# Kernel tuning notes

Hardware: AMD Instinct MI355X
Metric: run time of the kernel (lower is better)

Reference implementation:

```python
import jax, jax.numpy as jnp
import numpy as np

B, S, HID = 1, 2048, 4096
NH, KVH, D = 32, 8, 128
MAXP = 2048
EPS = 1e-6


def _rope_tables(max_pos, dim, base=10000.0):
    inv_freq = 1.0 / (base ** (np.arange(0, dim, 2, dtype=np.float32) / dim))
    t = np.arange(max_pos, dtype=np.float32)
    freqs = np.outer(t, inv_freq)                      # [max_pos, dim/2]
    emb = np.concatenate([freqs, freqs], axis=-1)      # [max_pos, dim]
    return jnp.asarray(np.cos(emb)), jnp.asarray(np.sin(emb))


def setup_inputs() -> dict:
    key = jax.random.key(0)
    ks = jax.random.split(key, 6)
    x = jax.random.normal(ks[0], (B, S, HID), jnp.float32)
    scale = 0.02
    wq = jax.random.normal(ks[1], (NH * D, HID), jnp.float32) * scale
    wk = jax.random.normal(ks[2], (KVH * D, HID), jnp.float32) * scale
    wv = jax.random.normal(ks[3], (KVH * D, HID), jnp.float32) * scale
    wo = jax.random.normal(ks[4], (NH * D, HID), jnp.float32).T * scale  # stored as [HID, NH*D] -> transpose back
    wo = jnp.asarray(jax.random.normal(ks[4], (HID, NH * D), jnp.float32) * scale)
    cos_table, sin_table = _rope_tables(MAXP, D)
    return {
        "x": x, "wq": wq, "wk": wk, "wv": wv, "wo": wo,
        "q_norm_w": jnp.ones((D,), jnp.float32),
        "k_norm_w": jnp.ones((D,), jnp.float32),
        "cos_table": cos_table, "sin_table": sin_table,
        "k_cache": jnp.zeros((1, B, MAXP, KVH, D), jnp.float32),
        "v_cache": jnp.zeros((1, B, MAXP, KVH, D), jnp.float32),
        "positions": jnp.arange(S, dtype=jnp.int32),
        "layer_idx": 0,
    }


def _rmsnorm(x, w):
    return w * (x * jax.lax.rsqrt(jnp.mean(x * x, axis=-1, keepdims=True) + EPS))


def _rope(x, cos, sin):
    # x: [B, H, S, D]; cos/sin: [1, 1, S, D]
    half = x.shape[-1] // 2
    x1, x2 = x[..., :half], x[..., half:]
    rotated = jnp.concatenate([-x2, x1], axis=-1)
    return x * cos + rotated * sin


def reference(x, wq, wk, wv, wo, q_norm_w, k_norm_w, cos_table, sin_table,
              k_cache, v_cache, positions, layer_idx):
    bsz, seq_len, _ = x.shape
    d = q_norm_w.shape[0]
    nh = wq.shape[0] // d
    kvh = wk.shape[0] // d
    g = nh // kvh

    q = (x @ wq.T).reshape(bsz, seq_len, nh, d).transpose(0, 2, 1, 3)    # [B,NH,S,D]
    k = (x @ wk.T).reshape(bsz, seq_len, kvh, d).transpose(0, 2, 1, 3)   # [B,KVH,S,D]
    v = (x @ wv.T).reshape(bsz, seq_len, kvh, d).transpose(0, 2, 1, 3)

    q = _rmsnorm(q, q_norm_w)
    k = _rmsnorm(k, k_norm_w)

    cos = cos_table[positions][None, None]  # [1,1,S,D]
    sin = sin_table[positions][None, None]
    q = _rope(q, cos, sin)
    k = _rope(k, cos, sin)

    # KV-cache scatter at dynamic positions (prefill: positions = arange(S))
    kc = k_cache[layer_idx].at[:, positions].set(k.transpose(0, 2, 1, 3))
    vc = v_cache[layer_idx].at[:, positions].set(v.transpose(0, 2, 1, 3))
    # K = max(positions)+1 == seq_len in this (prefill) setup; static for jit
    K = seq_len
    k_all = kc[:, :K].transpose(0, 2, 1, 3)   # [B,KVH,K,D]
    v_all = vc[:, :K].transpose(0, 2, 1, 3)

    # GQA: group query heads instead of repeat_interleave on K/V (same math)
    qg = q.reshape(bsz, kvh, g, seq_len, d)
    scale = 1.0 / jnp.sqrt(jnp.asarray(d, q.dtype))
    scores = jnp.einsum('bkgqd,bkld->bkgql', qg, k_all) * scale
    causal = jnp.tril(jnp.ones((seq_len, K), dtype=bool))
    scores = jnp.where(causal, scores, jnp.finfo(scores.dtype).min)
    attn = jax.nn.softmax(scores, axis=-1)
    out = jnp.einsum('bkgql,bkld->bkgqd', attn, v_all)
    out = out.reshape(bsz, nh, seq_len, d).transpose(0, 2, 1, 3).reshape(bsz, seq_len, nh * d)
    return out @ wo.T
```

## Files before the change

### kernel.cpp

```cpp
#include <hip/hip_runtime.h>

typedef unsigned short u16;
typedef unsigned int u32;
typedef __attribute__((ext_vector_type(8))) short bf16x8;
typedef __attribute__((ext_vector_type(4))) float f32x4;
struct __align__(8) us4 { u16 x, y, z, w; };

#define S_LEN 2048
#define HID   4096
#define NH    32
#define KVH   8
#define HD    128
#define MFMA16 __builtin_amdgcn_mfma_f32_16x16x32_bf16

__device__ inline u16 f2bf(float f) {
  u32 u = __float_as_uint(f);
  u32 r = (u + 0x7fffu + ((u >> 16) & 1u)) >> 16;
  return (u16)r;
}
__device__ inline float bf2f(u16 h) { return __uint_as_float(((u32)h) << 16); }

__device__ inline void gld_lds16(const void* g, void* l) {
  __builtin_amdgcn_global_load_lds(
      (const __attribute__((address_space(1))) u32*)g,
      (__attribute__((address_space(3))) u32*)l, 16, 0, 0);
}

__global__ __launch_bounds__(256)
void cvt_all(const float* __restrict__ x, const float* __restrict__ wq,
             const float* __restrict__ wk, const float* __restrict__ wv,
             u16* __restrict__ xb, u16* __restrict__ wqkvb) {
  int b = blockIdx.x;
  const float* in; u16* out; int base;
  if (b < 8192)       { in = x;  out = xb;                    base = b; }
  else if (b < 24576) { in = wq; out = wqkvb;                 base = b - 8192; }
  else if (b < 28672) { in = wk; out = wqkvb + 16777216;      base = b - 24576; }
  else                { in = wv; out = wqkvb + 20971520;      base = b - 28672; }
  size_t i = ((size_t)base * 256 + threadIdx.x) * 4;
  f32x4 v = *(const f32x4*)(in + i);
  us4 o;
  o.x = f2bf(v[0]); o.y = f2bf(v[1]); o.z = f2bf(v[2]); o.w = f2bf(v[3]);
  *(us4*)(out + i) = o;
}

__device__ __forceinline__ void stage_slab(const u16* __restrict__ src, int ldk,
                                           int rowBase, int k0, char* lslot,
                                           int t) {
  int rl = t >> 3;
  int c8 = ((t & 7) ^ (rl & 7)) * 8;
  gld_lds16(src + (size_t)(rowBase + rl) * ldk + k0 + c8, lslot + t * 16);
}

__device__ __forceinline__ void stage_half(const u16* __restrict__ src, int ldk,
                                           int rowBase, int k0, char* lslot,
                                           int t) {
  int rl = t >> 3;
  int c8 = ((t & 7) ^ (rl & 7)) * 8;
  gld_lds16(src + (size_t)(rowBase + rl) * ldk + k0 + c8, lslot + t * 16);
  gld_lds16(src + (size_t)(rowBase + 64 + rl) * ldk + k0 + c8,
            lslot + 8192 + t * 16);
}

__global__ __launch_bounds__(512, 2)
void gemm_qkv8(const u16* __restrict__ xb, const u16* __restrict__ wqkvb,
               u16* __restrict__ Qp, u16* __restrict__ Kp, u16* __restrict__ vt) {
  extern __shared__ char lds[];
  const int id = blockIdx.x;
  const int sw = (id & 7) * 32 + (id >> 3);
  const int by = sw >> 5, bx = sw & 31;
  const int m0 = by * 256, n0 = bx * 192;
  const int t = threadIdx.x;
  const int l = t & 63, w = t >> 6;
  const int l15 = l & 15, quad = l >> 4;
  const int wr = w >> 1, wcn = w & 1;
  char* ldsA = lds;
  char* ldsB = lds + 65536;
  const int swz0 = ((0 + quad) ^ (l15 & 7)) * 16;
  const int swz1 = ((4 + quad) ^ (l15 & 7)) * 16;
  const int aB0 = wr * 8192 + l15 * 128;
  const int bB0 = wcn * 12288 + l15 * 128;
  const int nt = HID / 64;

  f32x4 acc[4][6];
#pragma unroll
  for (int m = 0; m < 4; m++)
#pragma unroll
    for (int n = 0; n < 6; n++) acc[m][n] = (f32x4){0.f, 0.f, 0.f, 0.f};

#pragma unroll
  for (int s = 0; s < 3; s++) stage_slab(wqkvb, HID, n0 + s * 64, 0, ldsB + s * 8192, t);
#pragma unroll
  for (int s = 0; s < 4; s++) stage_slab(xb, HID, m0 + s * 64, 0, ldsA + s * 8192, t);
#pragma unroll
  for (int s = 0; s < 3; s++) stage_slab(wqkvb, HID, n0 + s * 64, 64, ldsB + 24576 + s * 8192, t);
  asm volatile("s_waitcnt vmcnt(3)" ::: "memory");
  __builtin_amdgcn_s_barrier();

  bf16x8 a[2][2], a2[2][2], b[3][2], b2[3][2];
#pragma unroll 1
  for (int tt = 0; tt < nt; ++tt) {
    const int d = tt & 1, dn = d ^ 1;
    const int aO = d * 32768 + aB0;
    const int bO = d * 24576 + bB0;
    const int k1 = (tt + 1) * 64, k2 = (tt + 2) * 64;
    const bool pf1 = (tt + 1 < nt), pf2 = (tt + 2 < nt);

#pragma unroll
    for (int m = 0; m < 2; m++) {
      a[m][0] = *(const bf16x8*)(ldsA + aO + m * 2048 + swz0);
      a[m][1] = *(const bf16x8*)(ldsA + aO + m * 2048 + swz1);
    }
#pragma unroll
    for (int n = 0; n < 3; n++) {
      b[n][0] = *(const bf16x8*)(ldsB + bO + n * 2048 + swz0);
      b[n][1] = *(const bf16x8*)(ldsB + bO + n * 2048 + swz1);
    }
    if (pf1) {
      stage_slab(xb, HID, m0,      k1, ldsA + dn * 32768,        t);
      stage_slab(xb, HID, m0 + 64, k1, ldsA + dn * 32768 + 8192, t);
    }
    __builtin_amdgcn_s_barrier();
    __builtin_amdgcn_s_setprio(1);
#pragma unroll
    for (int m = 0; m < 2; m++)
#pragma unroll
      for (int n = 0; n < 3; n++) {
        acc[m][n] = MFMA16(a[m][0], b[n][0], acc[m][n], 0, 0, 0);
        acc[m][n] = MFMA16(a[m][1], b[n][1], acc[m][n], 0, 0, 0);
      }
    __builtin_amdgcn_s_setprio(0);
    __builtin_amdgcn_s_barrier();

#pragma unroll
    for (int n = 0; n < 3; n++) {
      b2[n][0] = *(const bf16x8*)(ldsB + bO + (3 + n) * 2048 + swz0);
      b2[n][1] = *(const bf16x8*)(ldsB + bO + (3 + n) * 2048 + swz1);
    }
    if (pf1) {
      stage_slab(xb, HID, m0 + 128, k1, ldsA + dn * 32768 + 16384, t);
      stage_slab(xb, HID, m0 + 192, k1, ldsA + dn * 32768 + 24576, t);
    }
    __builtin_amdgcn_s_barrier();
    __builtin_amdgcn_s_setprio(1);
#pragma unroll
    for (int m = 0; m < 2; m++)
#pragma unroll
      for (int n = 0; n < 3; n++) {
        acc[m][3 + n] = MFMA16(a[m][0], b2[n][0], acc[m][3 + n], 0, 0, 0);
        acc[m][3 + n] = MFMA16(a[m][1], b2[n][1], acc[m][3 + n], 0, 0, 0);
      }
    __builtin_amdgcn_s_setprio(0);
    __builtin_amdgcn_s_barrier();

#pragma unroll
    for (int m = 0; m < 2; m++) {
      a2[m][0] = *(const bf16x8*)(ldsA + aO + (2 + m) * 2048 + swz0);
      a2[m][1] = *(const bf16x8*)(ldsA + aO + (2 + m) * 2048 + swz1);
    }
    if (pf2) {
#pragma unroll
      for (int s = 0; s < 3; s++)
        stage_slab(wqkvb, HID, n0 + s * 64, k2, ldsB + d * 24576 + s * 8192, t);
    }
    __builtin_amdgcn_s_barrier();
    __builtin_amdgcn_s_setprio(1);
#pragma unroll
    for (int m = 0; m < 2; m++)
#pragma unroll
      for (int n = 0; n < 3; n++) {
        acc[2 + m][n] = MFMA16(a2[m][0], b[n][0], acc[2 + m][n], 0, 0, 0);
        acc[2 + m][n] = MFMA16(a2[m][1], b[n][1], acc[2 + m][n], 0, 0, 0);
      }
#pragma unroll
    for (int m = 0; m < 2; m++)
#pragma unroll
      for (int n = 0; n < 3; n++) {
        acc[2 + m][3 + n] = MFMA16(a2[m][0], b2[n][0], acc[2 + m][3 + n], 0, 0, 0);
        acc[2 + m][3 + n] = MFMA16(a2[m][1], b2[n][1], acc[2 + m][3 + n], 0, 0, 0);
      }
    __builtin_amdgcn_s_setprio(0);
    if (pf1) {
      if (pf2) asm volatile("s_waitcnt vmcnt(3)" ::: "memory");
      else     asm volatile("s_waitcnt vmcnt(0)" ::: "memory");
      __builtin_amdgcn_s_barrier();
    }
  }

#pragma unroll
  for (int m = 0; m < 4; m++) {
    int row0 = m0 + wr * 64 + m * 16 + quad * 4;
#pragma unroll
    for (int n = 0; n < 6; n++) {
      int col = n0 + wcn * 96 + n * 16 + l15;
      if (col < 4096) {
#pragma unroll
        for (int r = 0; r < 4; r++)
          Qp[(size_t)(row0 + r) * HID + col] = f2bf(acc[m][n][r]);
      } else if (col < 5120) {
#pragma unroll
        for (int r = 0; r < 4; r++)
          Kp[(size_t)(row0 + r) * 1024 + (col - 4096)] = f2bf(acc[m][n][r]);
      } else {
        us4 v;
        v.x = f2bf(acc[m][n][0]); v.y = f2bf(acc[m][n][1]);
        v.z = f2bf(acc[m][n][2]); v.w = f2bf(acc[m][n][3]);
        *(us4*)(vt + (size_t)(col - 5120) * S_LEN + row0) = v;
      }
    }
  }
}

__device__ __forceinline__ void gemm256_core(
    const u16* __restrict__ A, const u16* __restrict__ W, int m0, int n0,
    int ldk, int kBeg, int kEnd, char* lds, f32x4 (&acc)[8][4]) {
  const int t = threadIdx.x;
  const int l = t & 63, w = t >> 6;
  const int l15 = l & 15, quad = l >> 4;
  const int wr = w >> 2, wcn = w & 3;
  const int nt = (kEnd - kBeg) >> 6;
  char* ldsA = lds;
  char* ldsB = lds + 65536;
  const int swz0 = ((0 + quad) ^ (l15 & 7)) * 16;
  const int swz1 = ((4 + quad) ^ (l15 & 7)) * 16;
  const int aB0 = wr * 16384 + l15 * 128;
  const int bB0 = wcn * 8192 + l15 * 128;

#pragma unroll
  for (int m = 0; m < 8; m++)
#pragma unroll
    for (int n = 0; n < 4; n++) acc[m][n] = (f32x4){0.f, 0.f, 0.f, 0.f};

  stage_half(W, ldk, n0,       kBeg, ldsB,         t);
  stage_half(W, ldk, n0 + 128, kBeg, ldsB + 16384, t);
  stage_half(A, ldk, m0,       kBeg, ldsA,         t);
  stage_half(A, ldk, m0 + 128, kBeg, ldsA + 16384, t);
  if (nt > 1) {
    stage_half(W, ldk, n0,       kBeg + 64, ldsB + 32768,         t);
    stage_half(W, ldk, n0 + 128, kBeg + 64, ldsB + 32768 + 16384, t);
    stage_half(A, ldk, m0,       kBeg + 64, ldsA + 32768,         t);
    stage_half(A, ldk, m0 + 128, kBeg + 64, ldsA + 32768 + 16384, t);
    asm volatile("s_waitcnt vmcnt(8)" ::: "memory");
  } else {
    asm volatile("s_waitcnt vmcnt(0)" ::: "memory");
  }
  __builtin_amdgcn_s_barrier();

  bf16x8 a[4][2], b[2][2], b2[2][2];
#pragma unroll 1
  for (int tt = 0; tt < nt; ++tt) {
    const int d = tt & 1;
    const int aO = d * 32768 + aB0;
    const int bO = d * 32768 + bB0;
    const int k2 = kBeg + (tt + 2) * 64;
    const bool pf = (tt + 2 < nt);

#pragma unroll
    for (int m = 0; m < 4; m++) {
      a[m][0] = *(const bf16x8*)(ldsA + aO + m * 2048 + swz0);
      a[m][1] = *(const bf16x8*)(ldsA + aO + m * 2048 + swz1);
    }
#pragma unroll
    for (int n = 0; n < 2; n++) {
      b[n][0] = *(const bf16x8*)(ldsB + bO + n * 2048 + swz0);
      b[n][1] = *(const bf16x8*)(ldsB + bO + n * 2048 + swz1);
    }
    __builtin_amdgcn_s_barrier();
    __builtin_amdgcn_s_setprio(1);
#pragma unroll
    for (int m = 0; m < 4; m++)
#pragma unroll
      for (int n = 0; n < 2; n++) {
        acc[m][n] = MFMA16(a[m][0], b[n][0], acc[m][n], 0, 0, 0);
        acc[m][n] = MFMA16(a[m][1], b[n][1], acc[m][n], 0, 0, 0);
      }
    __builtin_amdgcn_s_setprio(0);
    __builtin_amdgcn_s_barrier();

#pragma unroll
    for (int n = 0; n < 2; n++) {
      b2[n][0] = *(const bf16x8*)(ldsB + bO + (2 + n) * 2048 + swz0);
      b2[n][1] = *(const bf16x8*)(ldsB + bO + (2 + n) * 2048 + swz1);
    }
    __builtin_amdgcn_s_barrier();
    __builtin_amdgcn_s_setprio(1);
#pragma unroll
    for (int m = 0; m < 4; m++)
#pragma unroll
      for (int n = 0; n < 2; n++) {
        acc[m][2 + n] = MFMA16(a[m][0], b2[n][0], acc[m][2 + n], 0, 0, 0);
        acc[m][2 + n] = MFMA16(a[m][1], b2[n][1], acc[m][2 + n], 0, 0, 0);
      }
    __builtin_amdgcn_s_setprio(0);
    __builtin_amdgcn_s_barrier();

    if (pf) {
      stage_half(W, ldk, n0,       k2, ldsB + d * 32768,         t);
      stage_half(W, ldk, n0 + 128, k2, ldsB + d * 32768 + 16384, t);
    }
#pragma unroll
    for (int m = 0; m < 4; m++) {
      a[m][0] = *(const bf16x8*)(ldsA + aO + (4 + m) * 2048 + swz0);
      a[m][1] = *(const bf16x8*)(ldsA + aO + (4 + m) * 2048 + swz1);
    }
    __builtin_amdgcn_s_barrier();
    __builtin_amdgcn_s_setprio(1);
#pragma unroll
    for (int m = 0; m < 4; m++)
#pragma unroll
      for (int n = 0; n < 2; n++) {
        acc[4 + m][n] = MFMA16(a[m][0], b[n][0], acc[4 + m][n], 0, 0, 0);
        acc[4 + m][n] = MFMA16(a[m][1], b[n][1], acc[4 + m][n], 0, 0, 0);
      }
    __builtin_amdgcn_s_setprio(0);
    __builtin_amdgcn_s_barrier();

    if (pf) {
      stage_half(A, ldk, m0,       k2, ldsA + d * 32768,         t);
      stage_half(A, ldk, m0 + 128, k2, ldsA + d * 32768 + 16384, t);
    }
    __builtin_amdgcn_s_barrier();
    __builtin_amdgcn_s_setprio(1);
#pragma unroll
    for (int m = 0; m < 4; m++)
#pragma unroll
      for (int n = 0; n < 2; n++) {
        acc[4 + m][2 + n] = MFMA16(a[m][0], b2[n][0], acc[4 + m][2 + n], 0, 0, 0);
        acc[4 + m][2 + n] = MFMA16(a[m][1], b2[n][1], acc[4 + m][2 + n], 0, 0, 0);
      }
    __builtin_amdgcn_s_setprio(0);
    if (pf) asm volatile("s_waitcnt vmcnt(8)" ::: "memory");
    else    asm volatile("s_waitcnt vmcnt(0)" ::: "memory");
    __builtin_amdgcn_s_barrier();
  }
}

__global__ __launch_bounds__(512, 2)
void gemm_out8(const u16* __restrict__ ab, const u16* __restrict__ wob,
               float* __restrict__ O0, float* __restrict__ O1) {
  extern __shared__ char lds[];
  const int id = blockIdx.x;
  const int sw = (id & 7) * 32 + (id >> 3);
  const int z = sw >> 7, rem = sw & 127;
  const int by = rem >> 4, bx = rem & 15;
  float* Op = z ? O1 : O0;

  f32x4 acc[8][4];
  gemm256_core(ab, wob, by * 256, bx * 256, HID, z * 2048, z * 2048 + 2048, lds, acc);

  const int t = threadIdx.x, l = t & 63, w = t >> 6;
  const int l15 = l & 15, quad = l >> 4;
  const int wr = w >> 2, wcn = w & 3;
#pragma unroll
  for (int m = 0; m < 8; m++) {
    int row0 = by * 256 + wr * 128 + m * 16 + quad * 4;
#pragma unroll
    for (int n = 0; n < 4; n++) {
      int col = bx * 256 + wcn * 64 + n * 16 + l15;
#pragma unroll
      for (int r = 0; r < 4; r++)
        Op[(size_t)(row0 + r) * HID + col] = acc[m][n][r];
    }
  }
}

__global__ __launch_bounds__(256)
void reduce_out(const float* __restrict__ O0, const float* __restrict__ O1,
                float* __restrict__ outp) {
  size_t i = ((size_t)blockIdx.x * 256 + threadIdx.x) * 4;
  f32x4 a = *(const f32x4*)(O0 + i);
  f32x4 b = *(const f32x4*)(O1 + i);
  a[0] += b[0]; a[1] += b[1]; a[2] += b[2]; a[3] += b[3];
  *(f32x4*)(outp + i) = a;
}

__global__ __launch_bounds__(256)
void rope_all(const u16* __restrict__ Qp, const u16* __restrict__ Kp,
              const float* __restrict__ qnw, const float* __restrict__ knw,
              const float* __restrict__ cosT, const float* __restrict__ sinT,
              const int* __restrict__ pos, u16* __restrict__ qbh,
              u16* __restrict__ kbh) {
  const int b = blockIdx.x;
  const int t = threadIdx.x, w = t >> 6, l = t & 63;
  const u16* xr; const float* nw; u16* orow; int s;
  if (b < 16384) {
    int p = b * 4 + w;
    s = p >> 5; int h = p & 31;
    xr = Qp + (size_t)s * HID + h * HD;
    nw = qnw;
    orow = qbh + ((size_t)h * S_LEN + s) * HD;
  } else {
    int p = (b - 16384) * 4 + w;
    s = p >> 3; int h = p & 7;
    xr = Kp + (size_t)s * 1024 + h * HD;
    nw = knw;
    orow = kbh + ((size_t)h * S_LEN + s) * HD;
  }
  float x1 = bf2f(xr[l]);
  float x2 = bf2f(xr[l + 64]);
  float ss = x1 * x1 + x2 * x2;
#pragma unroll
  for (int m = 1; m < 64; m <<= 1) ss += __shfl_xor(ss, m);
  float rinv = rsqrtf(ss * (1.0f / 128.0f) + 1e-6f);
  float n1 = x1 * rinv * nw[l];
  float n2 = x2 * rinv * nw[l + 64];
  int ps = pos[s];
  float c1 = cosT[ps * HD + l], s1 = sinT[ps * HD + l];
  float c2 = cosT[ps * HD + l + 64], s2 = sinT[ps * HD + l + 64];
  float y1 = n1 * c1 - n2 * s1;
  float y2 = n2 * c2 + n1 * s2;
  orow[l] = f2bf(y1);
  orow[l + 64] = f2bf(y2);
}

__global__ __launch_bounds__(256)
void attn_fwd(const u16* __restrict__ qh, const u16* __restrict__ kbh,
              const u16* __restrict__ vth, u16* __restrict__ ab,
              const float* __restrict__ wo, u16* __restrict__ wob) {
  __shared__ __align__(16) u16 lK[64 * 128];
  __shared__ __align__(16) u16 lV[128 * 64];
  __shared__ __align__(16) u16 lP[4][16 * 72];
  const int t = threadIdx.x, w = t >> 6, l = t & 63;
  const int quad = l >> 4, l15 = l & 15;
  if (blockIdx.x >= NH) {
    int cb = (blockIdx.x - NH) * 32 + blockIdx.y;
    for (size_t i = (size_t)cb * 256 + t; i < 4194304; i += 98304) {
      size_t j = i * 4;
      f32x4 v = *(const f32x4*)(wo + j);
      us4 o;
      o.x = f2bf(v[0]); o.y = f2bf(v[1]); o.z = f2bf(v[2]); o.w = f2bf(v[3]);
      *(us4*)(wob + j) = o;
    }
    return;
  }
  const int h = blockIdx.x;
  const int qt = 31 - blockIdx.y;
  const int kvh = h >> 2;
  const int q0 = qt * 64;
  const int qrow = q0 + w * 16 + l15;

  bf16x8 qf[4];
#pragma unroll
  for (int ks = 0; ks < 4; ks++)
    qf[ks] = *(const bf16x8*)(qh + ((size_t)h * S_LEN + qrow) * HD + ks * 32 + quad * 8);

  f32x4 accO[8];
#pragma unroll
  for (int j = 0; j < 8; j++) accO[j] = (f32x4){0.f, 0.f, 0.f, 0.f};
  float m_cur = -3.0e38f, l_sum = 0.f;
  const float scale = 0.08838834764831845f;

  const int ntiles = qt + 1;
  for (int tt = 0; tt < ntiles; tt++) {
    const int c0 = tt * 64;
#pragma unroll
    for (int i = 0; i < 4; i++) {
      int Cc = i * 256 + t;
      int r = Cc >> 4, ch = Cc & 15;
      int gch = ch ^ (r & 15);
      gld_lds16(kbh + ((size_t)kvh * S_LEN + c0 + r) * HD + gch * 8, lK + Cc * 8);
    }
#pragma unroll
    for (int i = 0; i < 4; i++) {
      int Cc = i * 256 + t;
      int d = Cc >> 3, ch = Cc & 7;
      int gch = ch ^ (d & 7);
      gld_lds16(vth + ((size_t)kvh * HD + d) * S_LEN + c0 + gch * 8, lV + Cc * 8);
    }
    __syncthreads();

    f32x4 st[4];
#pragma unroll
    for (int i = 0; i < 4; i++) {
      f32x4 sa = (f32x4){0.f, 0.f, 0.f, 0.f};
      int r = i * 16 + l15;
#pragma unroll
      for (int ks = 0; ks < 4; ks++) {
        int lc = ks * 4 + quad;
        bf16x8 kf = *(const bf16x8*)(lK + r * 128 + ((lc ^ (r & 15)) * 8));
        sa = __builtin_amdgcn_mfma_f32_16x16x32_bf16(kf, qf[ks], sa, 0, 0, 0);
      }
      st[i] = sa;
    }

    float tmax = -3.0e38f;
#pragma unroll
    for (int i = 0; i < 4; i++) {
#pragma unroll
      for (int r = 0; r < 4; r++) {
        int kcol = c0 + i * 16 + quad * 4 + r;
        float v = st[i][r] * scale;
        v = (kcol <= qrow) ? v : -3.0e38f;
        st[i][r] = v;
        tmax = fmaxf(tmax, v);
      }
    }
    tmax = fmaxf(tmax, __shfl_xor(tmax, 16));
    tmax = fmaxf(tmax, __shfl_xor(tmax, 32));
    float m_new = fmaxf(m_cur, tmax);
    float alpha = __expf(m_cur - m_new);

    float psum = 0.f;
#pragma unroll
    for (int i = 0; i < 4; i++) {
      us4 pv;
      u16* pp = (u16*)&pv;
#pragma unroll
      for (int r = 0; r < 4; r++) {
        float pe = __expf(st[i][r] - m_new);
        psum += pe;
        pp[r] = f2bf(pe);
      }
      *(us4*)(&lP[w][l15 * 72 + i * 16 + quad * 4]) = pv;
    }
    psum += __shfl_xor(psum, 16);
    psum += __shfl_xor(psum, 32);
    l_sum = l_sum * alpha + psum;
    m_cur = m_new;

#pragma unroll
    for (int r = 0; r < 4; r++) {
      float ar = __shfl(alpha, quad * 4 + r);
#pragma unroll
      for (int j = 0; j < 8; j++) accO[j][r] *= ar;
    }

    bf16x8 pf[2];
#pragma unroll
    for (int ks = 0; ks < 2; ks++)
      pf[ks] = *(const bf16x8*)(&lP[w][l15 * 72 + ks * 32 + quad * 8]);
#pragma unroll
    for (int j = 0; j < 8; j++) {
      int d = j * 16 + l15;
#pragma unroll
      for (int ks = 0; ks < 2; ks++) {
        int lc = ks * 4 + quad;
        bf16x8 vf = *(const bf16x8*)(lV + d * 64 + ((lc ^ (d & 7)) * 8));
        accO[j] = __builtin_amdgcn_mfma_f32_16x16x32_bf16(pf[ks], vf, accO[j], 0, 0, 0);
      }
    }
    __syncthreads();
  }

  float linv = 1.0f / l_sum;
#pragma unroll
  for (int r = 0; r < 4; r++) {
    float lr = __shfl(linv, quad * 4 + r);
    int row = q0 + w * 16 + quad * 4 + r;
#pragma unroll
    for (int j = 0; j < 8; j++) {
      int col = h * HD + j * 16 + l15;
      ab[(size_t)row * HID + col] = f2bf(accO[j][r] * lr);
    }
  }
}

extern "C" void kernel_launch(void* const* d_in, const int* in_sizes, int n_in,
                              void* d_out, int out_size, void* d_ws, size_t ws_size,
                              hipStream_t stream) {
  const float* x    = (const float*)d_in[0];
  const float* wq   = (const float*)d_in[1];
  const float* wk   = (const float*)d_in[2];
  const float* wv   = (const float*)d_in[3];
  const float* wo   = (const float*)d_in[4];
  const float* qnw  = (const float*)d_in[5];
  const float* knw  = (const float*)d_in[6];
  const float* cosT = (const float*)d_in[7];
  const float* sinT = (const float*)d_in[8];
  const int* positions = (const int*)d_in[11];

  static int attr_done = 0;
  if (!attr_done) {
    hipFuncSetAttribute((const void*)gemm_qkv8,
                        hipFuncAttributeMaxDynamicSharedMemorySize, 114688);
    hipFuncSetAttribute((const void*)gemm_out8,
                        hipFuncAttributeMaxDynamicSharedMemorySize, 131072);
    attr_done = 1;
  }

  char* ws = (char*)d_ws;
  u16* xb    = (u16*)(ws + 0ULL);
  u16* wqkvb = (u16*)(ws + 16777216ULL);
  u16* wob   = (u16*)(ws + 67108864ULL);
  u16* Qp    = (u16*)(ws + 100663296ULL);
  u16* Kp    = (u16*)(ws + 117440512ULL);
  u16* vt    = (u16*)(ws + 121634816ULL);
  u16* qbh   = (u16*)(ws + 125829120ULL);
  u16* kbh   = (u16*)(ws + 142606336ULL);
  u16* ab    = (u16*)(ws + 146800640ULL);
  float* O0  = (float*)(ws + 0ULL);
  float* O1  = (float*)(ws + 33554432ULL);

  cvt_all<<<32768, 256, 0, stream>>>(x, wq, wk, wv, xb, wqkvb);

  gemm_qkv8<<<256, 512, 114688, stream>>>(xb, wqkvb, Qp, Kp, vt);

  rope_all<<<20480, 256, 0, stream>>>(Qp, Kp, qnw, knw, cosT, sinT, positions,
                                      qbh, kbh);

  attn_fwd<<<dim3(NH + 12, S_LEN / 64), 256, 0, stream>>>(qbh, kbh, vt, ab,
                                                          wo, wob);

  gemm_out8<<<256, 512, 131072, stream>>>(ab, wob, O0, O1);
  reduce_out<<<8192, 256, 0, stream>>>(O0, O1, (float*)d_out);
}
```

Before: 491.8 us.

## Double-buffer attention KV loads, lazy softmax rescale, replace split-K output GEMM

The attention kernel now double-buffers K/V tiles in dynamic LDS with async global-to-LDS prefetch two tiles ahead. It folds the softmax scale into Q during rope, applies the causal mask only on the diagonal tile, and skips the accumulator rescale when the running max grows by no more than a threshold. The output projection drops the split-K GEMM with its partial buffers and reduce kernel in favour of a single 256x128-tile GEMM that writes the final output directly. Together these aim to hide load latency, cut ALU work in the softmax loop, and remove a kernel launch plus extra memory traffic, at the cost of more LDS per block and a different tiling shape.

Result: no change. 483.8 us (-1.6%).

```diff
diff --git a/kernel.cpp b/kernel.cpp
--- a/kernel.cpp
+++ b/kernel.cpp
@@ -49,16 +49,6 @@
   int rl = t >> 3;
   int c8 = ((t & 7) ^ (rl & 7)) * 8;
   gld_lds16(src + (size_t)(rowBase + rl) * ldk + k0 + c8, lslot + t * 16);
-}
-
-__device__ __forceinline__ void stage_half(const u16* __restrict__ src, int ldk,
-                                           int rowBase, int k0, char* lslot,
-                                           int t) {
-  int rl = t >> 3;
-  int c8 = ((t & 7) ^ (rl & 7)) * 8;
-  gld_lds16(src + (size_t)(rowBase + rl) * ldk + k0 + c8, lslot + t * 16);
-  gld_lds16(src + (size_t)(rowBase + 64 + rl) * ldk + k0 + c8,
-            lslot + 8192 + t * 16);
 }
 
 __global__ __launch_bounds__(512, 2)
@@ -210,52 +200,52 @@
   }
 }
 
-__device__ __forceinline__ void gemm256_core(
-    const u16* __restrict__ A, const u16* __restrict__ W, int m0, int n0,
-    int ldk, int kBeg, int kEnd, char* lds, f32x4 (&acc)[8][4]) {
+__global__ __launch_bounds__(512, 2)
+void gemm_outF(const u16* __restrict__ ab, const u16* __restrict__ wob,
+               float* __restrict__ outp) {
+  extern __shared__ char lds[];
+  const int id = blockIdx.x;
+  const int sw = (id & 7) * 32 + (id >> 3);
+  const int by = sw >> 5, bx = sw & 31;
+  const int m0 = by * 256, n0 = bx * 128;
   const int t = threadIdx.x;
   const int l = t & 63, w = t >> 6;
   const int l15 = l & 15, quad = l >> 4;
-  const int wr = w >> 2, wcn = w & 3;
-  const int nt = (kEnd - kBeg) >> 6;
+  const int wr = w >> 1, wcn = w & 1;
   char* ldsA = lds;
   char* ldsB = lds + 65536;
   const int swz0 = ((0 + quad) ^ (l15 & 7)) * 16;
   const int swz1 = ((4 + quad) ^ (l15 & 7)) * 16;
-  const int aB0 = wr * 16384 + l15 * 128;
+  const int aB0 = wr * 8192 + l15 * 128;
   const int bB0 = wcn * 8192 + l15 * 128;
-
-#pragma unroll
-  for (int m = 0; m < 8; m++)
+  const int nt = HID / 64;
+
+  f32x4 acc[4][4];
+#pragma unroll
+  for (int m = 0; m < 4; m++)
 #pragma unroll
     for (int n = 0; n < 4; n++) acc[m][n] = (f32x4){0.f, 0.f, 0.f, 0.f};
 
-  stage_half(W, ldk, n0,       kBeg, ldsB,         t);
-  stage_half(W, ldk, n0 + 128, kBeg, ldsB + 16384, t);
-  stage_half(A, ldk, m0,       kBeg, ldsA,         t);
-  stage_half(A, ldk, m0 + 128, kBeg, ldsA + 16384, t);
-  if (nt > 1) {
-    stage_half(W, ldk, n0,       kBeg + 64, ldsB + 32768,         t);
-    stage_half(W, ldk, n0 + 128, kBeg + 64, ldsB + 32768 + 16384, t);
-    stage_half(A, ldk, m0,       kBeg + 64, ldsA + 32768,         t);
-    stage_half(A, ldk, m0 + 128, kBeg + 64, ldsA + 32768 + 16384, t);
-    asm volatile("s_waitcnt vmcnt(8)" ::: "memory");
-  } else {
-    asm volatile("s_waitcnt vmcnt(0)" ::: "memory");
-  }
+  stage_slab(wob, HID, n0,      0, ldsB,        t);
+  stage_slab(wob, HID, n0 + 64, 0, ldsB + 8192, t);
+#pragma unroll
+  for (int s = 0; s < 4; s++) stage_slab(ab, HID, m0 + s * 64, 0, ldsA + s * 8192, t);
+  stage_slab(wob, HID, n0,      64, ldsB + 16384,        t);
+  stage_slab(wob, HID, n0 + 64, 64, ldsB + 16384 + 8192, t);
+  asm volatile("s_waitcnt vmcnt(2)" ::: "memory");
   __builtin_amdgcn_s_barrier();
 
-  bf16x8 a[4][2], b[2][2], b2[2][2];
+  bf16x8 a[2][2], a2[2][2], b[2][2], b2[2][2];
 #pragma unroll 1
   for (int tt = 0; tt < nt; ++tt) {
-    const int d = tt & 1;
+    const int d = tt & 1, dn = d ^ 1;
     const int aO = d * 32768 + aB0;
-    const int bO = d * 32768 + bB0;
-    const int k2 = kBeg + (tt + 2) * 64;
-    const bool pf = (tt + 2 < nt);
-
-#pragma unroll
-    for (int m = 0; m < 4; m++) {
+    const int bO = d * 16384 + bB0;
+    const int k1 = (tt + 1) * 64, k2 = (tt + 2) * 64;
+    const bool pf1 = (tt + 1 < nt), pf2 = (tt + 2 < nt);
+
+#pragma unroll
+    for (int m = 0; m < 2; m++) {
       a[m][0] = *(const bf16x8*)(ldsA + aO + m * 2048 + swz0);
       a[m][1] = *(const bf16x8*)(ldsA + aO + m * 2048 + swz1);
     }
@@ -264,10 +254,14 @@
       b[n][0] = *(const bf16x8*)(ldsB + bO + n * 2048 + swz0);
       b[n][1] = *(const bf16x8*)(ldsB + bO + n * 2048 + swz1);
     }
+    if (pf1) {
+      stage_slab(ab, HID, m0,      k1, ldsA + dn * 32768,        t);
+      stage_slab(ab, HID, m0 + 64, k1, ldsA + dn * 32768 + 8192, t);
+    }
     __builtin_amdgcn_s_barrier();
     __builtin_amdgcn_s_setprio(1);
 #pragma unroll
-    for (int m = 0; m < 4; m++)
+    for (int m = 0; m < 2; m++)
 #pragma unroll
       for (int n = 0; n < 2; n++) {
         acc[m][n] = MFMA16(a[m][0], b[n][0], acc[m][n], 0, 0, 0);
@@ -281,10 +275,14 @@
       b2[n][0] = *(const bf16x8*)(ldsB + bO + (2 + n) * 2048 + swz0);
       b2[n][1] = *(const bf16x8*)(ldsB + bO + (2 + n) * 2048 + swz1);
     }
+    if (pf1) {
+      stage_slab(ab, HID, m0 + 128, k1, ldsA + dn * 32768 + 16384, t);
+      stage_slab(ab, HID, m0 + 192, k1, ldsA + dn * 32768 + 24576, t);
+    }
     __builtin_amdgcn_s_barrier();
     __builtin_amdgcn_s_setprio(1);
 #pragma unroll
-    for (int m = 0; m < 4; m++)
+    for (int m = 0; m < 2; m++)
 #pragma unroll
       for (int n = 0; n < 2; n++) {
         acc[m][2 + n] = MFMA16(a[m][0], b2[n][0], acc[m][2 + n], 0, 0, 0);
@@ -293,84 +291,50 @@
     __builtin_amdgcn_s_setprio(0);
     __builtin_amdgcn_s_barrier();
 
-    if (pf) {
-      stage_half(W, ldk, n0,       k2, ldsB + d * 32768,         t);
-      stage_half(W, ldk, n0 + 128, k2, ldsB + d * 32768 + 16384, t);
-    }
-#pragma unroll
-    for (int m = 0; m < 4; m++) {
-      a[m][0] = *(const bf16x8*)(ldsA + aO + (4 + m) * 2048 + swz0);
-      a[m][1] = *(const bf16x8*)(ldsA + aO + (4 + m) * 2048 + swz1);
+#pragma unroll
+    for (int m = 0; m < 2; m++) {
+      a2[m][0] = *(const bf16x8*)(ldsA + aO + (2 + m) * 2048 + swz0);
+      a2[m][1] = *(const bf16x8*)(ldsA + aO + (2 + m) * 2048 + swz1);
+    }
+    if (pf2) {
+      stage_slab(wob, HID, n0,      k2, ldsB + d * 16384,        t);
+      stage_slab(wob, HID, n0 + 64, k2, ldsB + d * 16384 + 8192, t);
     }
     __builtin_amdgcn_s_barrier();
     __builtin_amdgcn_s_setprio(1);
 #pragma unroll
-    for (int m = 0; m < 4; m++)
+    for (int m = 0; m < 2; m++)
 #pragma unroll
       for (int n = 0; n < 2; n++) {
-        acc[4 + m][n] = MFMA16(a[m][0], b[n][0], acc[4 + m][n], 0, 0, 0);
-        acc[4 + m][n] = MFMA16(a[m][1], b[n][1], acc[4 + m][n], 0, 0, 0);
+        acc[2 + m][n] = MFMA16(a2[m][0], b[n][0], acc[2 + m][n], 0, 0, 0);
+        acc[2 + m][n] = MFMA16(a2[m][1], b[n][1], acc[2 + m][n], 0, 0, 0);
+      }
+#pragma unroll
+    for (int m = 0; m < 2; m++)
+#pragma unroll
+      for (int n = 0; n < 2; n++) {
+        acc[2 + m][2 + n] = MFMA16(a2[m][0], b2[n][0], acc[2 + m][2 + n], 0, 0, 0);
+        acc[2 + m][2 + n] = MFMA16(a2[m][1], b2[n][1], acc[2 + m][2 + n], 0, 0, 0);
       }
     __builtin_amdgcn_s_setprio(0);
-    __builtin_amdgcn_s_barrier();
-
-    if (pf) {
-      stage_half(A, ldk, m0,       k2, ldsA + d * 32768,         t);
-      stage_half(A, ldk, m0 + 128, k2, ldsA + d * 32768 + 16384, t);
-    }
-    __builtin_amdgcn_s_barrier();
-    __builtin_amdgcn_s_setprio(1);
-#pragma unroll
-    for (int m = 0; m < 4; m++)
-#pragma unroll
-      for (int n = 0; n < 2; n++) {
-        acc[4 + m][2 + n] = MFMA16(a[m][0], b2[n][0], acc[4 + m][2 + n], 0, 0, 0);
-        acc[4 + m][2 + n] = MFMA16(a[m][1], b2[n][1], acc[4 + m][2 + n], 0, 0, 0);
-      }
-    __builtin_amdgcn_s_setprio(0);
-    if (pf) asm volatile("s_waitcnt vmcnt(8)" ::: "memory");
-    else    asm volatile("s_waitcnt vmcnt(0)" ::: "memory");
-    __builtin_amdgcn_s_barrier();
-  }
-}
-
-__global__ __launch_bounds__(512, 2)
-void gemm_out8(const u16* __restrict__ ab, const u16* __restrict__ wob,
-               float* __restrict__ O0, float* __restrict__ O1) {
-  extern __shared__ char lds[];
-  const int id = blockIdx.x;
-  const int sw = (id & 7) * 32 + (id >> 3);
-  const int z = sw >> 7, rem = sw & 127;
-  const int by = rem >> 4, bx = rem & 15;
-  float* Op = z ? O1 : O0;
-
-  f32x4 acc[8][4];
-  gemm256_core(ab, wob, by * 256, bx * 256, HID, z * 2048, z * 2048 + 2048, lds, acc);
-
-  const int t = threadIdx.x, l = t & 63, w = t >> 6;
-  const int l15 = l & 15, quad = l >> 4;
-  const int wr = w >> 2, wcn = w & 3;
-#pragma unroll
-  for (int m = 0; m < 8; m++) {
-    int row0 = by * 256 + wr * 128 + m * 16 + quad * 4;
+    if (pf1) {
+      if (pf2) asm volatile("s_waitcnt vmcnt(2)" ::: "memory");
+      else     asm volatile("s_waitcnt vmcnt(0)" ::: "memory");
+      __builtin_amdgcn_s_barrier();
+    }
+  }
+
+#pragma unroll
+  for (int m = 0; m < 4; m++) {
+    int row0 = m0 + wr * 64 + m * 16 + quad * 4;
 #pragma unroll
     for (int n = 0; n < 4; n++) {
-      int col = bx * 256 + wcn * 64 + n * 16 + l15;
+      int col = n0 + wcn * 64 + n * 16 + l15;
 #pragma unroll
       for (int r = 0; r < 4; r++)
-        Op[(size_t)(row0 + r) * HID + col] = acc[m][n][r];
-    }
-  }
-}
-
-__global__ __launch_bounds__(256)
-void reduce_out(const float* __restrict__ O0, const float* __restrict__ O1,
-                float* __restrict__ outp) {
-  size_t i = ((size_t)blockIdx.x * 256 + threadIdx.x) * 4;
-  f32x4 a = *(const f32x4*)(O0 + i);
-  f32x4 b = *(const f32x4*)(O1 + i);
-  a[0] += b[0]; a[1] += b[1]; a[2] += b[2]; a[3] += b[3];
-  *(f32x4*)(outp + i) = a;
+        outp[(size_t)(row0 + r) * HID + col] = acc[m][n][r];
+    }
+  }
 }
 
 __global__ __launch_bounds__(256)
@@ -382,18 +346,21 @@
   const int b = blockIdx.x;
   const int t = threadIdx.x, w = t >> 6, l = t & 63;
   const u16* xr; const float* nw; u16* orow; int s;
+  float sc;
   if (b < 16384) {
     int p = b * 4 + w;
     s = p >> 5; int h = p & 31;
     xr = Qp + (size_t)s * HID + h * HD;
     nw = qnw;
     orow = qbh + ((size_t)h * S_LEN + s) * HD;
+    sc = 0.08838834764831845f;
   } else {
     int p = (b - 16384) * 4 + w;
     s = p >> 3; int h = p & 7;
     xr = Kp + (size_t)s * 1024 + h * HD;
     nw = knw;
     orow = kbh + ((size_t)h * S_LEN + s) * HD;
+    sc = 1.0f;
   }
   float x1 = bf2f(xr[l]);
   float x2 = bf2f(xr[l + 64]);
@@ -408,17 +375,15 @@
   float c2 = cosT[ps * HD + l + 64], s2 = sinT[ps * HD + l + 64];
   float y1 = n1 * c1 - n2 * s1;
   float y2 = n2 * c2 + n1 * s2;
-  orow[l] = f2bf(y1);
-  orow[l + 64] = f2bf(y2);
+  orow[l] = f2bf(y1 * sc);
+  orow[l + 64] = f2bf(y2 * sc);
 }
 
 __global__ __launch_bounds__(256)
 void attn_fwd(const u16* __restrict__ qh, const u16* __restrict__ kbh,
               const u16* __restrict__ vth, u16* __restrict__ ab,
               const float* __restrict__ wo, u16* __restrict__ wob) {
-  __shared__ __align__(16) u16 lK[64 * 128];
-  __shared__ __align__(16) u16 lV[128 * 64];
-  __shared__ __align__(16) u16 lP[4][16 * 72];
+  extern __shared__ char alds[];
   const int t = threadIdx.x, w = t >> 6, l = t & 63;
   const int quad = l >> 4, l15 = l & 15;
   if (blockIdx.x >= NH) {
@@ -432,6 +397,9 @@
     }
     return;
   }
+  u16* lK = (u16*)alds;
+  u16* lV = (u16*)(alds + 32768);
+  u16* lP = (u16*)(alds + 65536) + w * 1152;
   const int h = blockIdx.x;
   const int qt = 31 - blockIdx.y;
   const int kvh = h >> 2;
@@ -447,26 +415,40 @@
 #pragma unroll
   for (int j = 0; j < 8; j++) accO[j] = (f32x4){0.f, 0.f, 0.f, 0.f};
   float m_cur = -3.0e38f, l_sum = 0.f;
-  const float scale = 0.08838834764831845f;
+
+#define STAGE_KV(TT, DB)                                                      \
+  do {                                                                        \
+    int c0s = (TT) * 64;                                                      \
+    _Pragma("unroll") for (int i = 0; i < 4; i++) {                           \
+      int Cc = i * 256 + t;                                                   \
+      int r = Cc >> 4, ch = Cc & 15;                                          \
+      int gch = ch ^ (r & 15);                                                \
+      gld_lds16(kbh + ((size_t)kvh * S_LEN + c0s + r) * HD + gch * 8,         \
+                lK + (DB) * 8192 + Cc * 8);                                   \
+    }                                                                         \
+    _Pragma("unroll") for (int i = 0; i < 4; i++) {                           \
+      int Cc = i * 256 + t;                                                   \
+      int dd = Cc >> 3, ch = Cc & 7;                                          \
+      int gch = ch ^ (dd & 7);                                                \
+      gld_lds16(vth + ((size_t)kvh * HD + dd) * S_LEN + c0s + gch * 8,        \
+                lV + (DB) * 8192 + Cc * 8);                                   \
+    }                                                                         \
+  } while (0)
 
   const int ntiles = qt + 1;
+  STAGE_KV(0, 0);
+  if (ntiles > 1) {
+    STAGE_KV(1, 1);
+    asm volatile("s_waitcnt vmcnt(8)" ::: "memory");
+  } else {
+    asm volatile("s_waitcnt vmcnt(0)" ::: "memory");
+  }
+  __builtin_amdgcn_s_barrier();
+
   for (int tt = 0; tt < ntiles; tt++) {
-    const int c0 = tt * 64;
-#pragma unroll
-    for (int i = 0; i < 4; i++) {
-      int Cc = i * 256 + t;
-      int r = Cc >> 4, ch = Cc & 15;
-      int gch = ch ^ (r & 15);
-      gld_lds16(kbh + ((size_t)kvh * S_LEN + c0 + r) * HD + gch * 8, lK + Cc * 8);
-    }
-#pragma unroll
-    for (int i = 0; i < 4; i++) {
-      int Cc = i * 256 + t;
-      int d = Cc >> 3, ch = Cc & 7;
-      int gch = ch ^ (d & 7);
-      gld_lds16(vth + ((size_t)kvh * HD + d) * S_LEN + c0 + gch * 8, lV + Cc * 8);
-    }
-    __syncthreads();
+    const int db = tt & 1;
+    const u16* lKd = lK + db * 8192;
+    const u16* lVd = lV + db * 8192;
 
     f32x4 st[4];
 #pragma unroll
@@ -476,28 +458,43 @@
 #pragma unroll
       for (int ks = 0; ks < 4; ks++) {
         int lc = ks * 4 + quad;
-        bf16x8 kf = *(const bf16x8*)(lK + r * 128 + ((lc ^ (r & 15)) * 8));
-        sa = __builtin_amdgcn_mfma_f32_16x16x32_bf16(kf, qf[ks], sa, 0, 0, 0);
+        bf16x8 kf = *(const bf16x8*)(lKd + r * 128 + ((lc ^ (r & 15)) * 8));
+        sa = MFMA16(kf, qf[ks], sa, 0, 0, 0);
       }
       st[i] = sa;
     }
 
+    if (tt == qt) {
+      const int c0 = tt * 64;
+#pragma unroll
+      for (int i = 0; i < 4; i++)
+#pragma unroll
+        for (int r = 0; r < 4; r++) {
+          int kcol = c0 + i * 16 + quad * 4 + r;
+          if (kcol > qrow) st[i][r] = -3.0e38f;
+        }
+    }
+
     float tmax = -3.0e38f;
 #pragma unroll
-    for (int i = 0; i < 4; i++) {
-#pragma unroll
-      for (int r = 0; r < 4; r++) {
-        int kcol = c0 + i * 16 + quad * 4 + r;
-        float v = st[i][r] * scale;
-        v = (kcol <= qrow) ? v : -3.0e38f;
-        st[i][r] = v;
-        tmax = fmaxf(tmax, v);
-      }
-    }
+    for (int i = 0; i < 4; i++)
+#pragma unroll
+      for (int r = 0; r < 4; r++) tmax = fmaxf(tmax, st[i][r]);
     tmax = fmaxf(tmax, __shfl_xor(tmax, 16));
     tmax = fmaxf(tmax, __shfl_xor(tmax, 32));
-    float m_new = fmaxf(m_cur, tmax);
-    float alpha = __expf(m_cur - m_new);
+
+    if (!__all(tmax <= m_cur + 8.0f)) {
+      float m_new = fmaxf(m_cur, tmax);
+      float alpha = __expf(m_cur - m_new);
+      l_sum *= alpha;
+#pragma unroll
+      for (int r = 0; r < 4; r++) {
+        float ar = __shfl(alpha, quad * 4 + r);
+#pragma unroll
+        for (int j = 0; j < 8; j++) accO[j][r] *= ar;
+      }
+      m_cur = m_new;
+    }
 
     float psum = 0.f;
 #pragma unroll
@@ -506,40 +503,40 @@
       u16* pp = (u16*)&pv;
 #pragma unroll
       for (int r = 0; r < 4; r++) {
-        float pe = __expf(st[i][r] - m_new);
+        float pe = __expf(st[i][r] - m_cur);
         psum += pe;
         pp[r] = f2bf(pe);
       }
-      *(us4*)(&lP[w][l15 * 72 + i * 16 + quad * 4]) = pv;
+      *(us4*)(lP + l15 * 72 + i * 16 + quad * 4) = pv;
     }
     psum += __shfl_xor(psum, 16);
     psum += __shfl_xor(psum, 32);
-    l_sum = l_sum * alpha + psum;
-    m_cur = m_new;
-
-#pragma unroll
-    for (int r = 0; r < 4; r++) {
-      float ar = __shfl(alpha, quad * 4 + r);
-#pragma unroll
-      for (int j = 0; j < 8; j++) accO[j][r] *= ar;
-    }
+    l_sum += psum;
 
     bf16x8 pf[2];
 #pragma unroll
     for (int ks = 0; ks < 2; ks++)
-      pf[ks] = *(const bf16x8*)(&lP[w][l15 * 72 + ks * 32 + quad * 8]);
+      pf[ks] = *(const bf16x8*)(lP + l15 * 72 + ks * 32 + quad * 8);
 #pragma unroll
     for (int j = 0; j < 8; j++) {
-      int d = j * 16 + l15;
+      int dd = j * 16 + l15;
 #pragma unroll
       for (int ks = 0; ks < 2; ks++) {
         int lc = ks * 4 + quad;
-        bf16x8 vf = *(const bf16x8*)(lV + d * 64 + ((lc ^ (d & 7)) * 8));
-        accO[j] = __builtin_amdgcn_mfma_f32_16x16x32_bf16(pf[ks], vf, accO[j], 0, 0, 0);
-      }
-    }
-    __syncthreads();
-  }
+        bf16x8 vf = *(const bf16x8*)(lVd + dd * 64 + ((lc ^ (dd & 7)) * 8));
+        accO[j] = MFMA16(pf[ks], vf, accO[j], 0, 0, 0);
+      }
+    }
+
+    __builtin_amdgcn_s_barrier();
+    if (tt + 2 < ntiles) STAGE_KV(tt + 2, db);
+    if (tt + 1 < ntiles) {
+      if (tt + 2 < ntiles) asm volatile("s_waitcnt vmcnt(8)" ::: "memory");
+      else                 asm volatile("s_waitcnt vmcnt(0)" ::: "memory");
+    }
+    __builtin_amdgcn_s_barrier();
+  }
+#undef STAGE_KV
 
   float linv = 1.0f / l_sum;
 #pragma unroll
@@ -572,8 +569,10 @@
   if (!attr_done) {
     hipFuncSetAttribute((const void*)gemm_qkv8,
                         hipFuncAttributeMaxDynamicSharedMemorySize, 114688);
-    hipFuncSetAttribute((const void*)gemm_out8,
-                        hipFuncAttributeMaxDynamicSharedMemorySize, 131072);
+    hipFuncSetAttribute((const void*)gemm_outF,
+                        hipFuncAttributeMaxDynamicSharedMemorySize, 98304);
+    hipFuncSetAttribute((const void*)attn_fwd,
+                        hipFuncAttributeMaxDynamicSharedMemorySize, 74752);
     attr_done = 1;
   }
 
@@ -587,8 +586,6 @@
   u16* qbh   = (u16*)(ws + 125829120ULL);
   u16* kbh   = (u16*)(ws + 142606336ULL);
   u16* ab    = (u16*)(ws + 146800640ULL);
-  float* O0  = (float*)(ws + 0ULL);
-  float* O1  = (float*)(ws + 33554432ULL);
 
   cvt_all<<<32768, 256, 0, stream>>>(x, wq, wk, wv, xb, wqkvb);
 
@@ -597,9 +594,8 @@
   rope_all<<<20480, 256, 0, stream>>>(Qp, Kp, qnw, knw, cosT, sinT, positions,
                                       qbh, kbh);
 
-  attn_fwd<<<dim3(NH + 12, S_LEN / 64), 256, 0, stream>>>(qbh, kbh, vt, ab,
-                                                          wo, wob);
-
-  gemm_out8<<<256, 512, 131072, stream>>>(ab, wob, O0, O1);
-  reduce_out<<<8192, 256, 0, stream>>>(O0, O1, (float*)d_out);
-}
+  attn_fwd<<<dim3(NH + 12, S_LEN / 64), 256, 74752, stream>>>(qbh, kbh, vt, ab,
+                                                              wo, wob);
+
+  gemm_outF<<<256, 512, 98304, stream>>>(ab, wob, (float*)d_out);
+}
```
